# Kernel optimization log

Measured on AMD Instinct MI355X. Metric: run time of the kernel, lower is better.

The kernel has to match this reference:

```python
import jax, jax.numpy as jnp
import numpy as np

NUM_HEADS = 16
HEAD_DIM = 128
EMBED = NUM_HEADS * HEAD_DIM  # 2048
BATCH, SEQ = 2, 2048


def setup_inputs() -> dict:
    key = jax.random.key(0)
    k1, k2 = jax.random.split(key)
    x = jax.random.normal(k1, (BATCH, SEQ, EMBED), dtype=jnp.float32)
    W = jax.random.normal(k2, (EMBED, 3 * EMBED), dtype=jnp.float32) * 0.02
    b = jnp.zeros((3 * EMBED,), dtype=jnp.float32)
    return {"x": x, "W": W, "b": b}


def _rotate_half(u):
    u1, u2 = jnp.split(u, 2, axis=-1)
    return jnp.concatenate([-u2, u1], axis=-1)


def reference(x, W, b):
    B, S, E = x.shape
    H, D = NUM_HEADS, HEAD_DIM
    # Fused QKV projection: [B,S,E] @ [E,3E] -> [B,S,3E]
    qkv = jnp.einsum('bse,ef->bsf', x, W) + b
    qkv = qkv.reshape(B, S, 3, H, D)
    q, k, v = qkv[:, :, 0], qkv[:, :, 1], qkv[:, :, 2]  # each [B,S,H,D]
    # Module's rotary embedding: sin/cos over arange(S*D), shared across heads
    t = jnp.arange(S * D, dtype=jnp.float32).reshape(1, S, 1, D)
    sin, cos = jnp.sin(t), jnp.cos(t)
    q = q * cos + _rotate_half(q) * sin
    k = k * cos + _rotate_half(k) * sin
    # Scaled dot-product attention over sequence, per head
    scale = 1.0 / jnp.sqrt(jnp.float32(D))
    attn = jnp.einsum('bqhd,bkhd->bhqk', q, k) * scale  # [B,H,S,S]
    w = jax.nn.softmax(attn, axis=-1)
    out = jnp.einsum('bhqk,bkhd->bqhd', w, v)  # [B,S,H,D]
    return out
```

## Files before the change

kernel.cpp:

```cpp
#include <hip/hip_runtime.h>
#include <stdint.h>

typedef unsigned short u16;
typedef __attribute__((ext_vector_type(8))) short bf16x8;
typedef __attribute__((ext_vector_type(4))) float f32x4;

#define NUM_B 2
#define SEQ   2048
#define SEQP  2080
#define NH    16
#define HD    128
#define EMB   2048
#define N3    6144
#define MM    4096
#define QT    64
#define WQ    32
#define KT    32
#define NTILE (SEQ / KT)

#define BM 128
#define BN 256
#define BK 64
#define NT_K (EMB / BK)

__device__ __forceinline__ u16 f2bf(float f) {
  union { float f; unsigned u; } c; c.f = f;
  return (u16)((c.u + 0x7FFFu + ((c.u >> 16) & 1u)) >> 16);
}
__device__ __forceinline__ void async16(const void* g, void* l) {
  __builtin_amdgcn_global_load_lds(
      (const __attribute__((address_space(1))) void*)g,
      (__attribute__((address_space(3))) void*)l, 16, 0, 0);
}

#define GBAR()   asm volatile("s_barrier" ::: "memory")
#define WLGKM0() asm volatile("s_waitcnt lgkmcnt(0)" ::: "memory")


__global__ void k_cvt_bf16(const float* __restrict__ in, u16* __restrict__ out, int n4) {
  int i = blockIdx.x * blockDim.x + threadIdx.x;
  if (i >= n4) return;
  const float4 v = ((const float4*)in)[i];
  ushort4 o;
  o.x = f2bf(v.x); o.y = f2bf(v.y); o.z = f2bf(v.z); o.w = f2bf(v.w);
  ((ushort4*)out)[i] = o;
}

__global__ void k_transpose_w(const float* __restrict__ W, u16* __restrict__ Wt) {
  __shared__ float t[32][33];
  int n0 = blockIdx.x * 32, k0 = blockIdx.y * 32;
  int tx = threadIdx.x, ty = threadIdx.y;
  #pragma unroll
  for (int i = ty; i < 32; i += 8)
    t[i][tx] = W[(size_t)(k0 + i) * N3 + n0 + tx];
  __syncthreads();
  #pragma unroll
  for (int i = ty; i < 32; i += 8)
    Wt[(size_t)(n0 + i) * EMB + k0 + tx] = f2bf(t[tx][i]);
}

__global__ void k_sincos(float2* __restrict__ tab) {
  int i = blockIdx.x * blockDim.x + threadIdx.x;
  double t = (double)i;
  tab[i] = make_float2((float)cos(t), (float)sin(t));
}

__global__ __launch_bounds__(512, 2) void k_gemm_qkv(
    const u16* __restrict__ xb, const u16* __restrict__ wt,
    const float* __restrict__ bias, const float2* __restrict__ tab,
    u16* __restrict__ qb, u16* __restrict__ kb, u16* __restrict__ vbt)
{
  __shared__ __align__(16) u16 lsA[3][BM * BK];
  __shared__ __align__(16) u16 lsB[2][BN * BK];
  const int tid = threadIdx.x;
  const int wave = tid >> 6, lane = tid & 63;
  const int lq = lane & 15, lr = lane >> 4;
  const int wr = wave >> 2, wc = wave & 3;
  const int m0 = blockIdx.y * BM, n0 = blockIdx.x * BN;

  auto stageA = [&](int t, int buf) {
    const int kt = t * BK;
    #pragma unroll
    for (int ii = 0; ii < 2; ++ii) {
      int s = ii * 512 + tid;
      int row = s >> 3, gq = (s & 7) ^ (row & 7);
      async16(xb + (size_t)(m0 + row) * EMB + kt + gq * 8, &lsA[buf][s * 8]);
    }
  };
  auto stageB = [&](int t, int buf, int half) {
    const int kt = t * BK;
    #pragma unroll
    for (int ii = 0; ii < 2; ++ii) {
      int s = ii * 512 + tid;
      int row = s >> 3, gq = (s & 7) ^ (row & 7);
      async16(wt + (size_t)(n0 + half * 128 + row) * EMB + kt + gq * 8,
              &lsB[buf][half * 8192 + s * 8]);
    }
  };

  f32x4 acc[4][4];
  #pragma unroll
  for (int i = 0; i < 4; ++i)
    #pragma unroll
    for (int j = 0; j < 4; ++j)
      acc[i][j] = f32x4{0.f, 0.f, 0.f, 0.f};

  int rbase[4];
  #pragma unroll
  for (int nf = 0; nf < 4; ++nf)
    rbase[nf] = ((wc >> 1) * 128 + (nf >> 1) * 64 + (wc & 1) * 32 + (nf & 1) * 16 + lq) * BK;
  const int aRow0 = (wr * 64 + lq) * BK;
  int qsw[2];
  qsw[0] = ((0 + lr) ^ (lq & 7)) * 8;
  qsw[1] = ((4 + lr) ^ (lq & 7)) * 8;

  stageA(0, 0); stageB(0, 0, 0); stageB(0, 0, 1);
  stageA(1, 1); stageB(1, 1, 0); stageB(1, 1, 1);
  asm volatile("s_waitcnt vmcnt(6)" ::: "memory");
  GBAR();

  int pa = 0;
  for (int t = 0; t < NT_K; ++t) {
    const u16* Ap = lsA[pa];
    const u16* Bp = lsB[t & 1];
    bf16x8 bfr[4][2];

    #pragma unroll
    for (int nf = 0; nf < 4; ++nf)
      #pragma unroll
      for (int kk = 0; kk < 2; ++kk)
        bfr[nf][kk] = *(const bf16x8*)(Bp + rbase[nf] + qsw[kk]);
    bf16x8 af0[2][2];
    #pragma unroll
    for (int mfl = 0; mfl < 2; ++mfl)
      #pragma unroll
      for (int kk = 0; kk < 2; ++kk)
        af0[mfl][kk] = *(const bf16x8*)(Ap + aRow0 + (mfl * 16) * BK + qsw[kk]);

    if (t + 2 < NT_K) {
      int pa2 = pa + 2; if (pa2 >= 3) pa2 -= 3;
      stageA(t + 2, pa2);
    }
    GBAR();
    WLGKM0();
    __builtin_amdgcn_s_setprio(1);
    #pragma unroll
    for (int kk = 0; kk < 2; ++kk)
      #pragma unroll
      for (int mfl = 0; mfl < 2; ++mfl)
        #pragma unroll
        for (int nf = 0; nf < 4; ++nf)
          acc[mfl][nf] = __builtin_amdgcn_mfma_f32_16x16x32_bf16(
              af0[mfl][kk], bfr[nf][kk], acc[mfl][nf], 0, 0, 0);
    __builtin_amdgcn_s_setprio(0);
    GBAR();

    bf16x8 af1[2][2];
    #pragma unroll
    for (int mfl = 0; mfl < 2; ++mfl)
      #pragma unroll
      for (int kk = 0; kk < 2; ++kk)
        af1[mfl][kk] = *(const bf16x8*)(Ap + aRow0 + (32 + mfl * 16) * BK + qsw[kk]);

    if (t + 2 < NT_K) {
      stageB(t + 2, t & 1, 0);
      stageB(t + 2, t & 1, 1);
      asm volatile("s_waitcnt vmcnt(6)" ::: "memory");
    } else if (t + 1 < NT_K) {
      asm volatile("s_waitcnt vmcnt(0)" ::: "memory");
    }
    GBAR();
    WLGKM0();
    __builtin_amdgcn_s_setprio(1);
    #pragma unroll
    for (int kk = 0; kk < 2; ++kk)
      #pragma unroll
      for (int mfl = 0; mfl < 2; ++mfl)
        #pragma unroll
        for (int nf = 0; nf < 4; ++nf)
          acc[2 + mfl][nf] = __builtin_amdgcn_mfma_f32_16x16x32_bf16(
              af1[mfl][kk], bfr[nf][kk], acc[2 + mfl][nf], 0, 0, 0);
    __builtin_amdgcn_s_setprio(0);
    GBAR();

    ++pa; if (pa >= 3) pa = 0;
  }

  const int w = n0 >> 11;
  const int h = ((n0 & 2047) >> 7) + (wc >> 1);
  float bb[4];
  int dloc[4];
  #pragma unroll
  for (int nf = 0; nf < 4; ++nf) {
    dloc[nf] = (nf >> 1) * 64 + (wc & 1) * 32 + (nf & 1) * 16 + lq;
    bb[nf] = bias[n0 + (wc >> 1) * 128 + dloc[nf]];
  }

  if (w == 2) {
    #pragma unroll
    for (int mfg = 0; mfg < 4; ++mfg) {
      int mg0 = m0 + wr * 64 + mfg * 16 + lr * 4;
      int b = mg0 >> 11, s0 = mg0 & 2047;
      #pragma unroll
      for (int nf = 0; nf < 4; ++nf) {
        int d = dloc[nf];
        ushort4 pk;
        pk.x = f2bf(acc[mfg][nf][0] + bb[nf]);
        pk.y = f2bf(acc[mfg][nf][1] + bb[nf]);
        pk.z = f2bf(acc[mfg][nf][2] + bb[nf]);
        pk.w = f2bf(acc[mfg][nf][3] + bb[nf]);
        *(ushort4*)(vbt + ((size_t)(b * NH + h) * HD + d) * SEQP + s0) = pk;
      }
    }
  } else {
    u16* basep = (w == 0) ? qb : kb;
    const float qs = (w == 0) ? 0.12751569843736827f : 1.0f;
    #pragma unroll
    for (int mfg = 0; mfg < 4; ++mfg)
      #pragma unroll
      for (int r = 0; r < 4; ++r) {
        int mg = m0 + wr * 64 + mfg * 16 + lr * 4 + r;
        int b = mg >> 11, s = mg & 2047;
        u16* dst = basep + ((size_t)(b * NH + h) * SEQ + s) * HD;
        #pragma unroll
        for (int nf = 0; nf < 2; ++nf) {
          int d1 = dloc[nf];
          float c1 = acc[mfg][nf][r]     + bb[nf];
          float c2 = acc[mfg][nf + 2][r] + bb[nf + 2];
          float2 s1 = tab[s * HD + d1];
          float2 s2 = tab[s * HD + d1 + 64];
          dst[d1]      = f2bf((c1 * s1.x - c2 * s1.y) * qs);
          dst[d1 + 64] = f2bf((c2 * s2.x + c1 * s2.y) * qs);
        }
      }
  }
}

__global__ __launch_bounds__(128, 2) void k_flash(
    const u16* __restrict__ qb, const u16* __restrict__ kb,
    const u16* __restrict__ vbt, float* __restrict__ out)
{
  __shared__ __align__(16) u16 lsK[2][KT * HD];
  __shared__ __align__(16) u16 lsV[2][HD * KT];
  __shared__ __align__(16) u16 lsP[2][WQ * KT];

  const int tid = threadIdx.x;
  const int wave = tid >> 6, lane = tid & 63;
  const int lq = lane & 15, lr = lane >> 4;
  const int i = blockIdx.x;
  const int xcd = i & 7, j = i >> 3;
  const int bh = xcd * 4 + (j >> 5);
  const int q0 = (j & 31) * QT;
  const u16* Qg = qb + ((size_t)bh * SEQ + q0 + wave * WQ) * HD;
  const u16* Kg = kb + (size_t)bh * SEQ * HD;
  const u16* Vg = vbt + (size_t)bh * HD * SEQP;

  auto stage = [&](int tile, int buf) {
    const int k0 = tile * KT;
    #pragma unroll
    for (int ii = 0; ii < 4; ++ii) {
      int c = tid + ii * 128;
      int key = c >> 4, grp = c & 15;
      async16(Kg + (size_t)(k0 + key) * HD + ((grp ^ (key & 7)) * 8), lsK[buf] + c * 8);
    }
    #pragma unroll
    for (int ii = 0; ii < 4; ++ii) {
      int c = tid + ii * 128;
      int d = c >> 2, g2 = c & 3;
      async16(Vg + (size_t)d * SEQP + k0 + ((g2 ^ ((d >> 1) & 3)) * 8), lsV[buf] + c * 8);
    }
  };

  stage(0, 0);

  bf16x8 qf[2][4];
  #pragma unroll
  for (int qq = 0; qq < 2; ++qq)
    #pragma unroll
    for (int ks = 0; ks < 4; ++ks)
      qf[qq][ks] = *(const bf16x8*)(Qg + (size_t)(qq * 16 + lq) * HD + ks * 32 + lr * 8);

  f32x4 acc_o[2][8];
  float lsum[2] = {0.f, 0.f};
  #pragma unroll
  for (int mb = 0; mb < 2; ++mb)
    #pragma unroll
    for (int nb = 0; nb < 8; ++nb) acc_o[mb][nb] = f32x4{0.f, 0.f, 0.f, 0.f};

  for (int t = 0; t < NTILE; ++t) {
    const int p = t & 1;
    __syncthreads();
    if (t + 1 < NTILE) stage(t + 1, 1 - p);

    f32x4 sacc[2][2];
    #pragma unroll
    for (int kbi = 0; kbi < 2; ++kbi)
      #pragma unroll
      for (int qq = 0; qq < 2; ++qq) sacc[kbi][qq] = f32x4{0.f, 0.f, 0.f, 0.f};
    #pragma unroll
    for (int ks = 0; ks < 4; ++ks) {
      bf16x8 kf[2];
      #pragma unroll
      for (int kbi = 0; kbi < 2; ++kbi) {
        int key = kbi * 16 + lq;
        int g = (ks * 4 + lr) ^ (key & 7);
        kf[kbi] = *(const bf16x8*)(lsK[p] + key * HD + g * 8);
      }
      #pragma unroll
      for (int kbi = 0; kbi < 2; ++kbi)
        #pragma unroll
        for (int qq = 0; qq < 2; ++qq)
          sacc[kbi][qq] = __builtin_amdgcn_mfma_f32_16x16x32_bf16(kf[kbi], qf[qq][ks], sacc[kbi][qq], 0, 0, 0);
    }

    #pragma unroll
    for (int kbi = 0; kbi < 2; ++kbi)
      #pragma unroll
      for (int qq = 0; qq < 2; ++qq) {
        float p0 = __builtin_amdgcn_exp2f(sacc[kbi][qq][0]);
        float p1 = __builtin_amdgcn_exp2f(sacc[kbi][qq][1]);
        float p2 = __builtin_amdgcn_exp2f(sacc[kbi][qq][2]);
        float p3 = __builtin_amdgcn_exp2f(sacc[kbi][qq][3]);
        lsum[qq] += (p0 + p1) + (p2 + p3);
        int row = qq * 16 + lq;
        int g = kbi * 4 + lr;
        int gp = g ^ (row & 6);
        uint2 pk;
        pk.x = (uint32_t)f2bf(p0) | ((uint32_t)f2bf(p1) << 16);
        pk.y = (uint32_t)f2bf(p2) | ((uint32_t)f2bf(p3) << 16);
        *(uint2*)(lsP[wave] + row * KT + gp * 4) = pk;
      }

    bf16x8 ap[2];
    #pragma unroll
    for (int mb = 0; mb < 2; ++mb) {
      int row = mb * 16 + lq;
      int gp = (2 * lr) ^ (row & 6);
      ap[mb] = *(const bf16x8*)(lsP[wave] + row * KT + gp * 4);
    }
    #pragma unroll
    for (int nb = 0; nb < 8; ++nb) {
      int d = nb * 16 + lq;
      int g2 = lr ^ ((d >> 1) & 3);
      bf16x8 bv = *(const bf16x8*)(lsV[p] + d * KT + g2 * 8);
      #pragma unroll
      for (int mb = 0; mb < 2; ++mb)
        acc_o[mb][nb] = __builtin_amdgcn_mfma_f32_16x16x32_bf16(ap[mb], bv[0] == bv[0] ? bv : bv, acc_o[mb][nb], 0, 0, 0);
    }
  }

  float inv[2];
  #pragma unroll
  for (int qq = 0; qq < 2; ++qq) {
    float s = lsum[qq];
    s += __shfl_xor(s, 16);
    s += __shfl_xor(s, 32);
    inv[qq] = 1.0f / s;
  }
  const int b = bh >> 4, h = bh & 15;
  #pragma unroll
  for (int mb = 0; mb < 2; ++mb)
    #pragma unroll
    for (int r = 0; r < 4; ++r) {
      float iv = __shfl(inv[mb], lr * 4 + r);
      int row = wave * WQ + mb * 16 + lr * 4 + r;
      int sq = q0 + row;
      float* op = out + (((size_t)b * SEQ + sq) * NH + h) * HD;
      #pragma unroll
      for (int nb = 0; nb < 8; ++nb)
        op[nb * 16 + lq] = acc_o[mb][nb][r] * iv;
    }
}


extern "C" void kernel_launch(void* const* d_in, const int* in_sizes, int n_in,
                              void* d_out, int out_size, void* d_ws, size_t ws_size,
                              hipStream_t stream) {
  (void)in_sizes; (void)n_in; (void)out_size; (void)ws_size;
  const float* x    = (const float*)d_in[0];
  const float* W    = (const float*)d_in[1];
  const float* bias = (const float*)d_in[2];
  float* out = (float*)d_out;

  char* p = (char*)d_ws;
  u16* xb  = (u16*)p;  p += (size_t)MM * EMB * 2;
  u16* wt  = (u16*)p;  p += (size_t)N3 * EMB * 2;
  u16* qb  = (u16*)p;  p += (size_t)NUM_B * NH * SEQ * HD * 2;
  u16* kb  = (u16*)p;  p += (size_t)NUM_B * NH * SEQ * HD * 2;
  u16* vbt = (u16*)p;  p += (size_t)NUM_B * NH * HD * SEQP * 2;
  float2* tab = (float2*)p;

  k_cvt_bf16<<<(MM * EMB / 4 + 255) / 256, 256, 0, stream>>>(x, xb, MM * EMB / 4);
  k_transpose_w<<<dim3(N3 / 32, EMB / 32), dim3(32, 8), 0, stream>>>(W, wt);
  k_sincos<<<(SEQ * HD) / 256, 256, 0, stream>>>(tab);
  k_gemm_qkv<<<dim3(N3 / BN, MM / BM), 512, 0, stream>>>(xb, wt, bias, tab, qb, kb, vbt);
  k_flash<<<SEQ / QT * NUM_B * NH, 128, 0, stream>>>(qb, kb, vbt, out);
}
```

Baseline: 260.9 us.

## Split QKV GEMM k-loop phases by K-half and triple-buffer B tiles

```diff
diff --git a/kernel.cpp b/kernel.cpp
--- a/kernel.cpp
+++ b/kernel.cpp
@@ -71,7 +71,7 @@
     u16* __restrict__ qb, u16* __restrict__ kb, u16* __restrict__ vbt)
 {
   __shared__ __align__(16) u16 lsA[3][BM * BK];
-  __shared__ __align__(16) u16 lsB[2][BN * BK];
+  __shared__ __align__(16) u16 lsB[3][BN * BK];
   const int tid = threadIdx.x;
   const int wave = tid >> 6, lane = tid & 63;
   const int lq = lane & 15, lr = lane >> 4;
@@ -122,49 +122,41 @@
   int pa = 0;
   for (int t = 0; t < NT_K; ++t) {
     const u16* Ap = lsA[pa];
-    const u16* Bp = lsB[t & 1];
-    bf16x8 bfr[4][2];
-
+    const u16* Bp = lsB[pa];
+    int pa2 = pa + 2; if (pa2 >= 3) pa2 -= 3;
+
+    bf16x8 af0[4], bf0[4];
     #pragma unroll
     for (int nf = 0; nf < 4; ++nf)
-      #pragma unroll
-      for (int kk = 0; kk < 2; ++kk)
-        bfr[nf][kk] = *(const bf16x8*)(Bp + rbase[nf] + qsw[kk]);
-    bf16x8 af0[2][2];
-    #pragma unroll
-    for (int mfl = 0; mfl < 2; ++mfl)
-      #pragma unroll
-      for (int kk = 0; kk < 2; ++kk)
-        af0[mfl][kk] = *(const bf16x8*)(Ap + aRow0 + (mfl * 16) * BK + qsw[kk]);
-
-    if (t + 2 < NT_K) {
-      int pa2 = pa + 2; if (pa2 >= 3) pa2 -= 3;
-      stageA(t + 2, pa2);
-    }
+      bf0[nf] = *(const bf16x8*)(Bp + rbase[nf] + qsw[0]);
+    #pragma unroll
+    for (int mfg = 0; mfg < 4; ++mfg)
+      af0[mfg] = *(const bf16x8*)(Ap + aRow0 + (mfg * 16) * BK + qsw[0]);
+
+    if (t + 2 < NT_K) stageA(t + 2, pa2);
     GBAR();
     WLGKM0();
     __builtin_amdgcn_s_setprio(1);
     #pragma unroll
-    for (int kk = 0; kk < 2; ++kk)
-      #pragma unroll
-      for (int mfl = 0; mfl < 2; ++mfl)
-        #pragma unroll
-        for (int nf = 0; nf < 4; ++nf)
-          acc[mfl][nf] = __builtin_amdgcn_mfma_f32_16x16x32_bf16(
-              af0[mfl][kk], bfr[nf][kk], acc[mfl][nf], 0, 0, 0);
+    for (int mfg = 0; mfg < 4; ++mfg)
+      #pragma unroll
+      for (int nf = 0; nf < 4; ++nf)
+        acc[mfg][nf] = __builtin_amdgcn_mfma_f32_16x16x32_bf16(
+            af0[mfg], bf0[nf], acc[mfg][nf], 0, 0, 0);
     __builtin_amdgcn_s_setprio(0);
     GBAR();
 
-    bf16x8 af1[2][2];
-    #pragma unroll
-    for (int mfl = 0; mfl < 2; ++mfl)
-      #pragma unroll
-      for (int kk = 0; kk < 2; ++kk)
-        af1[mfl][kk] = *(const bf16x8*)(Ap + aRow0 + (32 + mfl * 16) * BK + qsw[kk]);
+    bf16x8 af1[4], bf1[4];
+    #pragma unroll
+    for (int nf = 0; nf < 4; ++nf)
+      bf1[nf] = *(const bf16x8*)(Bp + rbase[nf] + qsw[1]);
+    #pragma unroll
+    for (int mfg = 0; mfg < 4; ++mfg)
+      af1[mfg] = *(const bf16x8*)(Ap + aRow0 + (mfg * 16) * BK + qsw[1]);
 
     if (t + 2 < NT_K) {
-      stageB(t + 2, t & 1, 0);
-      stageB(t + 2, t & 1, 1);
+      stageB(t + 2, pa2, 0);
+      stageB(t + 2, pa2, 1);
       asm volatile("s_waitcnt vmcnt(6)" ::: "memory");
     } else if (t + 1 < NT_K) {
       asm volatile("s_waitcnt vmcnt(0)" ::: "memory");
@@ -173,13 +165,11 @@
     WLGKM0();
     __builtin_amdgcn_s_setprio(1);
     #pragma unroll
-    for (int kk = 0; kk < 2; ++kk)
-      #pragma unroll
-      for (int mfl = 0; mfl < 2; ++mfl)
-        #pragma unroll
-        for (int nf = 0; nf < 4; ++nf)
-          acc[2 + mfl][nf] = __builtin_amdgcn_mfma_f32_16x16x32_bf16(
-              af1[mfl][kk], bfr[nf][kk], acc[2 + mfl][nf], 0, 0, 0);
+    for (int mfg = 0; mfg < 4; ++mfg)
+      #pragma unroll
+      for (int nf = 0; nf < 4; ++nf)
+        acc[mfg][nf] = __builtin_amdgcn_mfma_f32_16x16x32_bf16(
+            af1[mfg], bf1[nf], acc[mfg][nf], 0, 0, 0);
     __builtin_amdgcn_s_setprio(0);
     GBAR();
 
```

After: 257.7 us. Within noise of the previous version (-1.2%).
